# Performance work log

Hardware: AMD Instinct MI355X
Metric: run time of the kernel (lower is better)

## Reference

```python
import jax, jax.numpy as jnp
import numpy as np

BATCH = 1
SEQ = 2048
HIDDEN = 2048
NUM_HEADS = 16
NUM_KV_HEADS = 4
HEAD_DIM = HIDDEN // NUM_HEADS  # 128
KV_GROUPS = NUM_HEADS // NUM_KV_HEADS  # 4
MIN_WIN, MAX_WIN = 64, 512


def _adaptive_window_mask(key):
    # Per-query adaptive window size in [MIN_WIN, MAX_WIN); causal + windowed.
    win = jax.random.randint(key, (SEQ,), MIN_WIN, MAX_WIN)  # [S]
    i = jnp.arange(SEQ)[:, None]  # query pos
    j = jnp.arange(SEQ)[None, :]  # key pos
    mask = (j <= i) & (j > i - win[:, None])  # diagonal always True
    return jnp.broadcast_to(mask[None, None], (BATCH, 1, SEQ, SEQ))


def setup_inputs() -> dict:
    key = jax.random.key(0)
    ks = jax.random.split(key, 6)
    std = 0.02
    return {
        "hidden_states": jax.random.normal(ks[0], (BATCH, SEQ, HIDDEN), jnp.float32),
        "attention_mask": _adaptive_window_mask(ks[1]),
        "Wq": jax.random.normal(ks[2], (HIDDEN, NUM_HEADS * HEAD_DIM), jnp.float32) * std,
        "Wk": jax.random.normal(ks[3], (HIDDEN, NUM_KV_HEADS * HEAD_DIM), jnp.float32) * std,
        "Wv": jax.random.normal(ks[4], (HIDDEN, NUM_KV_HEADS * HEAD_DIM), jnp.float32) * std,
        "Wo": jax.random.normal(ks[5], (NUM_HEADS * HEAD_DIM, HIDDEN), jnp.float32) * std,
    }


def reference(hidden_states, attention_mask, Wq, Wk, Wv, Wo):
    B, S, H = hidden_states.shape
    # Projections (no bias, LLaMA-style)
    q = (hidden_states @ Wq).reshape(B, S, NUM_HEADS, HEAD_DIM).transpose(0, 2, 1, 3)
    k = (hidden_states @ Wk).reshape(B, S, NUM_KV_HEADS, HEAD_DIM).transpose(0, 2, 1, 3)
    v = (hidden_states @ Wv).reshape(B, S, NUM_KV_HEADS, HEAD_DIM).transpose(0, 2, 1, 3)
    # GQA: repeat_interleave along head dim
    k = jnp.repeat(k, KV_GROUPS, axis=1)  # [B, NUM_HEADS, S, D]
    v = jnp.repeat(v, KV_GROUPS, axis=1)
    scale = 1.0 / np.sqrt(HEAD_DIM).astype(np.float32)
    scores = jnp.einsum("bhqd,bhkd->bhqk", q, k) * scale  # [B, H, S, S]
    # bool mask: masked positions get -inf (matches masked_fill_(-inf) + add)
    scores = jnp.where(attention_mask, scores, -jnp.inf)
    attn = jax.nn.softmax(scores, axis=-1)
    out = jnp.einsum("bhqk,bhkd->bhqd", attn, v)
    out = out.transpose(0, 2, 1, 3).reshape(B, S, H) @ Wo
    return out
```

## Files before the change

kernel.cpp:

```cpp
#include <hip/hip_runtime.h>
#include <hip/hip_bf16.h>

typedef __attribute__((ext_vector_type(4)))  float f32x4;
typedef __attribute__((ext_vector_type(16))) float f32x16;
typedef __attribute__((ext_vector_type(8)))  short bf16x8;
typedef unsigned short u16;
typedef unsigned int   u32;
typedef unsigned long long u64;
typedef __attribute__((ext_vector_type(2))) u32 u32x2;
typedef __attribute__((ext_vector_type(4))) u32 u32x4;

#define S_LEN 2048
#define HID   2048
#define NH    16
#define NKV   4
#define HD    128
#define DKV   512
#define QK_SCALE 0.08838834764831845f

__device__ __forceinline__ u16 f2bf(float x) {
    u32 u = __builtin_bit_cast(u32, x);
    u32 r = (u + 0x7fffu + ((u >> 16) & 1u)) >> 16;
    return (u16)r;
}
__device__ __forceinline__ float bf2f(u16 b) {
    u32 u = ((u32)b) << 16;
    return __builtin_bit_cast(float, u);
}
__device__ __forceinline__ void gload_lds16(const void* g, void* l) {
    __builtin_amdgcn_global_load_lds(
        (const __attribute__((address_space(1))) u32*)g,
        (__attribute__((address_space(3))) u32*)l, 16, 0, 0);
}
__device__ __forceinline__ u32x4 pack8(const u16* o) {
    u32x4 r;
    r[0] = (u32)o[0] | ((u32)o[1] << 16);
    r[1] = (u32)o[2] | ((u32)o[3] << 16);
    r[2] = (u32)o[4] | ((u32)o[5] << 16);
    r[3] = (u32)o[6] | ((u32)o[7] << 16);
    return r;
}

__device__ __forceinline__ void plswap(u32 a, u32 b, u32& x0, u32& x1) {
#if __has_builtin(__builtin_amdgcn_permlane32_swap)
    u32x2 r = __builtin_amdgcn_permlane32_swap(a, b, false, false);
    x0 = r[0]; x1 = r[1];
#else
    u32 oa = (u32)__shfl_xor((int)a, 32);
    u32 ob = (u32)__shfl_xor((int)b, 32);
    int hi = (threadIdx.x & 63) >> 5;
    x0 = hi ? ob : a;
    x1 = hi ? b : oa;
#endif
}
__device__ __forceinline__ float pairmax32(float v) {
    u32 x0, x1; plswap(__builtin_bit_cast(u32, v), __builtin_bit_cast(u32, v), x0, x1);
    return fmaxf(__builtin_bit_cast(float, x0), __builtin_bit_cast(float, x1));
}
__device__ __forceinline__ float pairsum32(float v) {
    u32 x0, x1; plswap(__builtin_bit_cast(u32, v), __builtin_bit_cast(u32, v), x0, x1);
    return __builtin_bit_cast(float, x0) + __builtin_bit_cast(float, x1);
}

#define NTQ 1024
#define NTK 256
#define NTV 256
#define NTO 1024
#define NT_W (NTQ + NTK + NTV + NTO)
#define NB_CVT 1024
#define NB_START 128
#define NB_PREP (NT_W + NB_CVT + NB_START)

__global__ __launch_bounds__(256) void prep_kernel(
        const u32* __restrict__ X, const unsigned char* __restrict__ mask,
        const void* __restrict__ Wq, const void* __restrict__ Wk,
        const void* __restrict__ Wv, const void* __restrict__ Wo,
        u16* __restrict__ Xbf, u16* __restrict__ WqT, u16* __restrict__ WkT,
        u16* __restrict__ WvT, u16* __restrict__ WoT, int* __restrict__ start)
{
    __shared__ float tile[64][65];
    const int tid = threadIdx.x, lane = tid & 63, wave = tid >> 6;

    int big = 0, nz = 0;
    #pragma unroll
    for (int i = 0; i < 4; i++) {
        u32 v = X[lane + i * 64];
        u16 lo = (u16)(v & 0xffffu);
        int e = (lo >> 7) & 0xff;
        big |= (e >= 0x83);
        nz  |= (lo != 0);
    }
    const int isf32 = (__ballot(big) != 0ull || __ballot(nz) == 0ull) ? 1 : 0;

    const int b = blockIdx.x;
    if (b < NT_W) {
        const void* src; u16* dst; int N, ty;
        if (b < NTQ)                  { src = Wq; dst = WqT; N = 2048; ty = b; }
        else if (b < NTQ + NTK)       { src = Wk; dst = WkT; N = 512;  ty = b - NTQ; }
        else if (b < NTQ + NTK + NTV) { src = Wv; dst = WvT; N = 512;  ty = b - NTQ - NTK; }
        else                          { src = Wo; dst = WoT; N = 2048; ty = b - NTQ - NTK - NTV; }
        const int K = 2048;
        const int ntx = N >> 6;
        const int k0 = (ty / ntx) << 6, n0 = (ty % ntx) << 6;
        const int kk = tid >> 4, cg = (tid & 15) << 2;
        if (isf32) {
            const float* W = (const float*)src;
            #pragma unroll
            for (int it = 0; it < 4; it++) {
                f32x4 v = *(const f32x4*)(W + (size_t)(k0 + kk + it * 16) * N + n0 + cg);
                tile[kk + it * 16][cg + 0] = v[0]; tile[kk + it * 16][cg + 1] = v[1];
                tile[kk + it * 16][cg + 2] = v[2]; tile[kk + it * 16][cg + 3] = v[3];
            }
        } else {
            const u16* W = (const u16*)src;
            #pragma unroll
            for (int it = 0; it < 4; it++) {
                u64 v = *(const u64*)(W + (size_t)(k0 + kk + it * 16) * N + n0 + cg);
                tile[kk + it * 16][cg + 0] = bf2f((u16)(v));
                tile[kk + it * 16][cg + 1] = bf2f((u16)(v >> 16));
                tile[kk + it * 16][cg + 2] = bf2f((u16)(v >> 32));
                tile[kk + it * 16][cg + 3] = bf2f((u16)(v >> 48));
            }
        }
        __syncthreads();
        const int nn = tid >> 2;
        #pragma unroll
        for (int it = 0; it < 2; it++) {
            int kof = ((tid & 3) + it * 4) << 3;
            u16 ob[8];
            #pragma unroll
            for (int j = 0; j < 8; j++) ob[j] = f2bf(tile[kof + j][nn]);
            *(u32x4*)(dst + (size_t)(n0 + nn) * K + k0 + kof) = pack8(ob);
        }
    } else if (b < NT_W + NB_CVT) {
        const long base = ((long)(b - NT_W) * 256 + tid) * 16;
        u16 ob[16];
        if (isf32) {
            const float* p = (const float*)X;
            #pragma unroll
            for (int c = 0; c < 4; c++) {
                f32x4 v = *(const f32x4*)(p + base + c * 4);
                ob[c * 4 + 0] = f2bf(v[0]); ob[c * 4 + 1] = f2bf(v[1]);
                ob[c * 4 + 2] = f2bf(v[2]); ob[c * 4 + 3] = f2bf(v[3]);
            }
        } else {
            const u16* p = (const u16*)X;
            #pragma unroll
            for (int j = 0; j < 16; j++) ob[j] = p[base + j];
        }
        *(u32x4*)(Xbf + base) = pack8(ob);
        *(u32x4*)(Xbf + base + 8) = pack8(ob + 8);
    } else {
        const int b3 = b - NT_W - NB_CVT;
        const bool w1 = (mask[2049] != 0);
        #pragma unroll
        for (int rr = 0; rr < 4; rr++) {
            const int r = b3 * 16 + wave * 4 + rr;
            int cnt = 0;
            if (w1) {
                const u32* row = (const u32*)(mask + (size_t)r * S_LEN);
                #pragma unroll
                for (int i = 0; i < 8; i++) {
                    u32 v = row[lane + i * 64];
                    cnt += (int)(((v & 0x01010101u) * 0x01010101u) >> 24);
                }
            } else {
                const u32* row = (const u32*)mask + (size_t)r * S_LEN;
                #pragma unroll
                for (int i = 0; i < 32; i++) cnt += (row[lane + i * 64] != 0);
            }
            #pragma unroll
            for (int off = 32; off; off >>= 1) cnt += __shfl_down(cnt, off);
            if (lane == 0) start[r] = r + 1 - cnt;
        }
    }
}

__global__ __launch_bounds__(256) void gemm_qkv_kernel(
        const u16* __restrict__ A, const u16* __restrict__ BT,
        u16* __restrict__ Qo, u16* __restrict__ Ko, u16* __restrict__ Vto)
{
    __shared__ char smem[49152];
    const int tid = threadIdx.x;
    const int wave = tid >> 6, lane = tid & 63, g = lane >> 4, q = lane & 15;
    const int wr = wave >> 1, wc = wave & 1;
    const int gx = gridDim.x, nwg = gx * gridDim.y;
    const int wg = blockIdx.x + blockIdx.y * gx;
    const int swz = (wg & 7) * (nwg >> 3) + (wg >> 3);
    const int m0 = (swz / gx) * 128, n0 = (swz % gx) * 64;
    const int K = HID;

    f32x4 acc[4][2];
    #pragma unroll
    for (int i = 0; i < 4; i++)
        #pragma unroll
        for (int j = 0; j < 2; j++) acc[i][j] = (f32x4){0.f, 0.f, 0.f, 0.f};

    auto stage = [&](int kt, int b) {
        const int kbase = kt << 6;
        #pragma unroll
        for (int it = 0; it < 4; ++it) {
            int idx = it * 256 + tid;
            int row = idx >> 3, ch = idx & 7;
            int sch = ch ^ (row & 7);
            gload_lds16(A + (size_t)(m0 + row) * K + kbase + sch * 8,
                        smem + b * 16384 + idx * 16);
        }
        #pragma unroll
        for (int it = 0; it < 2; ++it) {
            int idx = it * 256 + tid;
            int row = idx >> 3, ch = idx & 7;
            int sch = ch ^ (row & 7);
            gload_lds16(BT + (size_t)(n0 + row) * K + kbase + sch * 8,
                        smem + 32768 + b * 8192 + idx * 16);
        }
    };

    const int KT = K >> 6;
    stage(0, 0);
    __syncthreads();
    int cur = 0;
    for (int kt = 0; kt < KT; ++kt) {
        if (kt + 1 < KT) stage(kt + 1, cur ^ 1);
        const char* sa = smem + cur * 16384;
        const char* sb = smem + 32768 + cur * 8192;
        #pragma unroll
        for (int kk = 0; kk < 2; ++kk) {
            bf16x8 af[4], bfr[2];
            #pragma unroll
            for (int i = 0; i < 4; i++) {
                int ra = wr * 64 + i * 16 + q;
                af[i] = *(const bf16x8*)(sa + ra * 128 + (((kk * 4 + g) ^ (ra & 7)) * 16));
            }
            #pragma unroll
            for (int j = 0; j < 2; j++) {
                int rb = wc * 32 + j * 16 + q;
                bfr[j] = *(const bf16x8*)(sb + rb * 128 + (((kk * 4 + g) ^ (rb & 7)) * 16));
            }
            #pragma unroll
            for (int i = 0; i < 4; i++)
                #pragma unroll
                for (int j = 0; j < 2; j++)
                    acc[i][j] = __builtin_amdgcn_mfma_f32_16x16x32_bf16(af[i], bfr[j], acc[i][j], 0, 0, 0);
        }
        __syncthreads();
        cur ^= 1;
    }
    #pragma unroll
    for (int i = 0; i < 4; i++) {
        #pragma unroll
        for (int j = 0; j < 2; j++) {
            #pragma unroll
            for (int r = 0; r < 4; r++) {
                int m = m0 + wr * 64 + i * 16 + g * 4 + r;
                int n = n0 + wc * 32 + j * 16 + q;
                float v = acc[i][j][r];
                if (n0 < 2048)      Qo[(size_t)m * HID + n] = f2bf(v * QK_SCALE);
                else if (n0 < 2560) Ko[(size_t)m * DKV + (n - 2048)] = f2bf(v);
                else                Vto[(size_t)(n - 2560) * S_LEN + m] = f2bf(v);
            }
        }
    }
}

template <int MODE>
__global__ __launch_bounds__(256) void gemm_bt_kernel(
        const u16* __restrict__ A, const u16* __restrict__ BT, void* __restrict__ Cv,
        int M, int N, int K, float scale)
{
    __shared__ char smem[49152];
    const int tid = threadIdx.x;
    const int wave = tid >> 6, lane = tid & 63, g = lane >> 4, q = lane & 15;
    const int wr = wave >> 1, wc = wave & 1;
    const int gx = gridDim.x, nwg = gx * gridDim.y;
    const int wg = blockIdx.x + blockIdx.y * gx;
    const int swz = (nwg & 7) == 0 ? ((wg & 7) * (nwg >> 3) + (wg >> 3)) : wg;
    const int m0 = (swz / gx) * 128, n0 = (swz % gx) * 64;

    f32x4 acc[4][2];
    #pragma unroll
    for (int i = 0; i < 4; i++)
        #pragma unroll
        for (int j = 0; j < 2; j++) acc[i][j] = (f32x4){0.f, 0.f, 0.f, 0.f};

    auto stage = [&](int kt, int b) {
        const int kbase = kt << 6;
        #pragma unroll
        for (int it = 0; it < 4; ++it) {
            int idx = it * 256 + tid;
            int row = idx >> 3, ch = idx & 7;
            int sch = ch ^ (row & 7);
            gload_lds16(A + (size_t)(m0 + row) * K + kbase + sch * 8,
                        smem + b * 16384 + idx * 16);
        }
        #pragma unroll
        for (int it = 0; it < 2; ++it) {
            int idx = it * 256 + tid;
            int row = idx >> 3, ch = idx & 7;
            int sch = ch ^ (row & 7);
            gload_lds16(BT + (size_t)(n0 + row) * K + kbase + sch * 8,
                        smem + 32768 + b * 8192 + idx * 16);
        }
    };

    const int KT = K >> 6;
    stage(0, 0);
    __syncthreads();
    int cur = 0;
    for (int kt = 0; kt < KT; ++kt) {
        if (kt + 1 < KT) stage(kt + 1, cur ^ 1);
        const char* sa = smem + cur * 16384;
        const char* sb = smem + 32768 + cur * 8192;
        #pragma unroll
        for (int kk = 0; kk < 2; ++kk) {
            bf16x8 af[4], bfr[2];
            #pragma unroll
            for (int i = 0; i < 4; i++) {
                int ra = wr * 64 + i * 16 + q;
                af[i] = *(const bf16x8*)(sa + ra * 128 + (((kk * 4 + g) ^ (ra & 7)) * 16));
            }
            #pragma unroll
            for (int j = 0; j < 2; j++) {
                int rb = wc * 32 + j * 16 + q;
                bfr[j] = *(const bf16x8*)(sb + rb * 128 + (((kk * 4 + g) ^ (rb & 7)) * 16));
            }
            #pragma unroll
            for (int i = 0; i < 4; i++)
                #pragma unroll
                for (int j = 0; j < 2; j++)
                    acc[i][j] = __builtin_amdgcn_mfma_f32_16x16x32_bf16(af[i], bfr[j], acc[i][j], 0, 0, 0);
        }
        __syncthreads();
        cur ^= 1;
    }
    #pragma unroll
    for (int i = 0; i < 4; i++) {
        #pragma unroll
        for (int j = 0; j < 2; j++) {
            #pragma unroll
            for (int r = 0; r < 4; r++) {
                int m = m0 + wr * 64 + i * 16 + g * 4 + r;
                int n = n0 + wc * 32 + j * 16 + q;
                float v = acc[i][j][r] * scale;
                if (MODE == 3) ((float*)Cv)[(size_t)m * N + n] = v;
                else           ((u16*)Cv)[(size_t)m * N + n] = f2bf(v);
            }
        }
    }
}

__global__ __launch_bounds__(256, 1) void attn_kernel(
        const u16* __restrict__ Q, const u16* __restrict__ Kb,
        const u16* __restrict__ Vt, u16* __restrict__ O, const int* __restrict__ start)
{
    const int tid = threadIdx.x, wave = tid >> 6, lane = tid & 63;
    const int q = lane & 31, hi = lane >> 5;
    const int h = blockIdx.y, hk = h >> 2;
    const int r0 = blockIdx.x * 128 + wave * 32;
    const int qrow = r0 + q;

    const u16* qp = Q + (size_t)qrow * HID + h * HD + hi * 8;
    bf16x8 Qf[8];
    #pragma unroll
    for (int kc = 0; kc < 8; kc++) Qf[kc] = *(const bf16x8*)(qp + kc * 16);

    const int startq = start[qrow];
    int jlo = startq;
    #pragma unroll
    for (int off = 1; off < 32; off <<= 1) jlo = min(jlo, __shfl_xor(jlo, off));
    const int jend = r0 + 31;

    float m = -INFINITY, l = 0.f;
    f32x16 o[4];
    #pragma unroll
    for (int dt = 0; dt < 4; dt++) o[dt] = (f32x16){};

    for (int j0 = (jlo & ~31); j0 <= jend; j0 += 32) {
        const u16* kp = Kb + (size_t)(j0 + q) * DKV + hk * HD + hi * 8;
        bf16x8 Kf[8];
        #pragma unroll
        for (int kc = 0; kc < 8; kc++) Kf[kc] = *(const bf16x8*)(kp + kc * 16);
        const u16* vp = Vt + (size_t)(hk * HD + q) * S_LEN + j0 + hi * 8;
        bf16x8 Vf[8];
        #pragma unroll
        for (int dt = 0; dt < 4; dt++)
            #pragma unroll
            for (int c = 0; c < 2; c++)
                Vf[dt * 2 + c] = *(const bf16x8*)(vp + (size_t)dt * 32 * S_LEN + c * 16);

        f32x16 s = (f32x16){};
        #pragma unroll
        for (int kc = 0; kc < 8; kc++)
            s = __builtin_amdgcn_mfma_f32_32x32x16_bf16(Kf[kc], Qf[kc], s, 0, 0, 0);

        float sv[16];
        float pmax = -INFINITY;
        #pragma unroll
        for (int r = 0; r < 16; r++) {
            int j = j0 + (r & 3) + 8 * (r >> 2) + 4 * hi;
            float x = (j <= qrow && j >= startq) ? s[r] : -INFINITY;
            sv[r] = x;
            pmax = fmaxf(pmax, x);
        }
        pmax = pairmax32(pmax);

        bool defer = __all(pmax <= m + 8.f);
        float mnew = m;
        if (!defer) {
            mnew = fmaxf(m, pmax);
            float corr = (m == -INFINITY) ? 0.f : __expf(m - mnew);
            l *= corr;
            #pragma unroll
            for (int dt = 0; dt < 4; dt++)
                #pragma unroll
                for (int r = 0; r < 16; r++) o[dt][r] *= corr;
            m = mnew;
        }

        float ps = 0.f;
        u16 pb[16];
        #pragma unroll
        for (int r = 0; r < 16; r++) {
            float p = (sv[r] == -INFINITY) ? 0.f : __expf(sv[r] - mnew);
            ps += p;
            pb[r] = f2bf(p);
        }
        l += pairsum32(ps);

        u32 w[8];
        #pragma unroll
        for (int i = 0; i < 8; i++) w[i] = (u32)pb[2 * i] | ((u32)pb[2 * i + 1] << 16);
        u32 x0, x1, y0, y1;
        plswap(w[0], w[2], x0, x1); plswap(w[1], w[3], y0, y1);
        u32x4 c0w = {x0, y0, x1, y1};
        bf16x8 P0 = __builtin_bit_cast(bf16x8, c0w);
        plswap(w[4], w[6], x0, x1); plswap(w[5], w[7], y0, y1);
        u32x4 c1w = {x0, y0, x1, y1};
        bf16x8 P1 = __builtin_bit_cast(bf16x8, c1w);

        #pragma unroll
        for (int dt = 0; dt < 4; dt++) {
            o[dt] = __builtin_amdgcn_mfma_f32_32x32x16_bf16(Vf[dt * 2 + 0], P0, o[dt], 0, 0, 0);
            o[dt] = __builtin_amdgcn_mfma_f32_32x32x16_bf16(Vf[dt * 2 + 1], P1, o[dt], 0, 0, 0);
        }
    }

    float inv = 1.0f / l;
    u16* op = O + (size_t)qrow * HID + h * HD + 4 * hi;
    #pragma unroll
    for (int dt = 0; dt < 4; dt++) {
        #pragma unroll
        for (int rb = 0; rb < 16; rb += 4) {
            u64 wd = (u64)f2bf(o[dt][rb + 0] * inv) |
                     ((u64)f2bf(o[dt][rb + 1] * inv) << 16) |
                     ((u64)f2bf(o[dt][rb + 2] * inv) << 32) |
                     ((u64)f2bf(o[dt][rb + 3] * inv) << 48);
            *(u64*)(op + dt * 32 + 2 * rb) = wd;
        }
    }
}

extern "C" void kernel_launch(void* const* d_in, const int* in_sizes, int n_in,
                              void* d_out, int out_size, void* d_ws, size_t ws_size,
                              hipStream_t stream)
{
    char* ws = (char*)d_ws;
    const size_t MB = 1024 * 1024;
    int* start = (int*)(ws + 1024);
    u16* Xbf = (u16*)(ws + 16384);
    u16* WqT = (u16*)(ws + 16384 + 8 * MB);
    u16* WkT = (u16*)(ws + 16384 + 16 * MB);
    u16* WvT = (u16*)(ws + 16384 + 18 * MB);
    u16* WoT = (u16*)(ws + 16384 + 20 * MB);
    u16* Qbf = (u16*)(ws + 16384 + 28 * MB);
    u16* Kbf = (u16*)(ws + 16384 + 36 * MB);
    u16* Vtb = (u16*)(ws + 16384 + 38 * MB);
    u16* Obf = (u16*)(ws + 16384 + 40 * MB);

    const void* X  = d_in[0];
    const unsigned char* mask = (const unsigned char*)d_in[1];
    const void* Wq = d_in[2];
    const void* Wk = d_in[3];
    const void* Wv = d_in[4];
    const void* Wo = d_in[5];

    prep_kernel<<<NB_PREP, 256, 0, stream>>>(
        (const u32*)X, mask, Wq, Wk, Wv, Wo, Xbf, WqT, WkT, WvT, WoT, start);

    gemm_qkv_kernel<<<dim3(48, HID / 128), 256, 0, stream>>>(Xbf, WqT, Qbf, Kbf, Vtb);

    attn_kernel<<<dim3(S_LEN / 128, NH), 256, 0, stream>>>(Qbf, Kbf, Vtb, Obf, start);

    gemm_bt_kernel<3><<<dim3(HID / 64, S_LEN / 128), 256, 0, stream>>>(Obf, WoT, d_out, S_LEN, HID, HID, 1.f);
}
```

Before: 118.3 us.

## Triple-buffer LDS in GEMM kernels with vmcnt-based partial waits

Moves the QKV and output-projection GEMMs from double to triple buffering in LDS, prefetching two K-tiles ahead. The full __syncthreads drain is replaced by s_waitcnt vmcnt(6) plus a raw barrier, so the next tile's loads stay in flight while the current tile is computed. This is meant to hide global-load latency better. In exchange, LDS per workgroup grows from 48KB to 72KB, which can cut occupancy, and correctness now depends on the hand-counted outstanding loads per stage.

```diff
diff --git a/kernel.cpp b/kernel.cpp
--- a/kernel.cpp
+++ b/kernel.cpp
@@ -180,7 +180,7 @@
         const u16* __restrict__ A, const u16* __restrict__ BT,
         u16* __restrict__ Qo, u16* __restrict__ Ko, u16* __restrict__ Vto)
 {
-    __shared__ char smem[49152];
+    __shared__ char smem[73728];
     const int tid = threadIdx.x;
     const int wave = tid >> 6, lane = tid & 63, g = lane >> 4, q = lane & 15;
     const int wr = wave >> 1, wc = wave & 1;
@@ -212,18 +212,12 @@
             int row = idx >> 3, ch = idx & 7;
             int sch = ch ^ (row & 7);
             gload_lds16(BT + (size_t)(n0 + row) * K + kbase + sch * 8,
-                        smem + 32768 + b * 8192 + idx * 16);
+                        smem + 49152 + b * 8192 + idx * 16);
         }
     };
-
-    const int KT = K >> 6;
-    stage(0, 0);
-    __syncthreads();
-    int cur = 0;
-    for (int kt = 0; kt < KT; ++kt) {
-        if (kt + 1 < KT) stage(kt + 1, cur ^ 1);
-        const char* sa = smem + cur * 16384;
-        const char* sb = smem + 32768 + cur * 8192;
+    auto compute = [&](int b) {
+        const char* sa = smem + b * 16384;
+        const char* sb = smem + 49152 + b * 8192;
         #pragma unroll
         for (int kk = 0; kk < 2; ++kk) {
             bf16x8 af[4], bfr[2];
@@ -243,9 +237,23 @@
                 for (int j = 0; j < 2; j++)
                     acc[i][j] = __builtin_amdgcn_mfma_f32_16x16x32_bf16(af[i], bfr[j], acc[i][j], 0, 0, 0);
         }
-        __syncthreads();
-        cur ^= 1;
-    }
+    };
+
+    const int KT = K >> 6;
+    stage(0, 0); stage(1, 1);
+    asm volatile("s_waitcnt vmcnt(6)" ::: "memory");
+    __builtin_amdgcn_s_barrier();
+    for (int kt = 0; kt < KT - 2; ++kt) {
+        stage(kt + 2, (kt + 2) % 3);
+        compute(kt % 3);
+        asm volatile("s_waitcnt vmcnt(6)" ::: "memory");
+        __builtin_amdgcn_s_barrier();
+    }
+    compute((KT - 2) % 3);
+    asm volatile("s_waitcnt vmcnt(0)" ::: "memory");
+    __builtin_amdgcn_s_barrier();
+    compute((KT - 1) % 3);
+
     #pragma unroll
     for (int i = 0; i < 4; i++) {
         #pragma unroll
@@ -268,7 +276,7 @@
         const u16* __restrict__ A, const u16* __restrict__ BT, void* __restrict__ Cv,
         int M, int N, int K, float scale)
 {
-    __shared__ char smem[49152];
+    __shared__ char smem[73728];
     const int tid = threadIdx.x;
     const int wave = tid >> 6, lane = tid & 63, g = lane >> 4, q = lane & 15;
     const int wr = wave >> 1, wc = wave & 1;
@@ -299,18 +307,12 @@
             int row = idx >> 3, ch = idx & 7;
             int sch = ch ^ (row & 7);
             gload_lds16(BT + (size_t)(n0 + row) * K + kbase + sch * 8,
-                        smem + 32768 + b * 8192 + idx * 16);
+                        smem + 49152 + b * 8192 + idx * 16);
         }
     };
-
-    const int KT = K >> 6;
-    stage(0, 0);
-    __syncthreads();
-    int cur = 0;
-    for (int kt = 0; kt < KT; ++kt) {
-        if (kt + 1 < KT) stage(kt + 1, cur ^ 1);
-        const char* sa = smem + cur * 16384;
-        const char* sb = smem + 32768 + cur * 8192;
+    auto compute = [&](int b) {
+        const char* sa = smem + b * 16384;
+        const char* sb = smem + 49152 + b * 8192;
         #pragma unroll
         for (int kk = 0; kk < 2; ++kk) {
             bf16x8 af[4], bfr[2];
@@ -330,9 +332,23 @@
                 for (int j = 0; j < 2; j++)
                     acc[i][j] = __builtin_amdgcn_mfma_f32_16x16x32_bf16(af[i], bfr[j], acc[i][j], 0, 0, 0);
         }
-        __syncthreads();
-        cur ^= 1;
-    }
+    };
+
+    const int KT = K >> 6;
+    stage(0, 0); stage(1, 1);
+    asm volatile("s_waitcnt vmcnt(6)" ::: "memory");
+    __builtin_amdgcn_s_barrier();
+    for (int kt = 0; kt < KT - 2; ++kt) {
+        stage(kt + 2, (kt + 2) % 3);
+        compute(kt % 3);
+        asm volatile("s_waitcnt vmcnt(6)" ::: "memory");
+        __builtin_amdgcn_s_barrier();
+    }
+    compute((KT - 2) % 3);
+    asm volatile("s_waitcnt vmcnt(0)" ::: "memory");
+    __builtin_amdgcn_s_barrier();
+    compute((KT - 1) % 3);
+
     #pragma unroll
     for (int i = 0; i < 4; i++) {
         #pragma unroll
```

Measured after the change: 122.7 us. 1.04x slower.

## Load QKV GEMM B operand directly into registers, bypassing LDS

Applied to the files above, without the earlier changes.

The QKV projection GEMM no longer stages the weight (B) tile through shared memory. Each wave loads its B fragments straight from global memory into registers, double-buffered in two register sets, while A is still staged through LDS. The main loop is unrolled by two to alternate between the register buffers. This cuts LDS footprint from 48KB to 32KB and removes the B-side LDS writes and reads, which may raise occupancy. In exchange it adds register pressure, and each B row is fetched by both waves sharing the same wc, doubling global B traffic through cache.

```diff
diff --git a/kernel.cpp b/kernel.cpp
--- a/kernel.cpp
+++ b/kernel.cpp
@@ -180,7 +180,7 @@
         const u16* __restrict__ A, const u16* __restrict__ BT,
         u16* __restrict__ Qo, u16* __restrict__ Ko, u16* __restrict__ Vto)
 {
-    __shared__ char smem[49152];
+    __shared__ char smem[32768];
     const int tid = threadIdx.x;
     const int wave = tid >> 6, lane = tid & 63, g = lane >> 4, q = lane & 15;
     const int wr = wave >> 1, wc = wave & 1;
@@ -196,7 +196,9 @@
         #pragma unroll
         for (int j = 0; j < 2; j++) acc[i][j] = (f32x4){0.f, 0.f, 0.f, 0.f};
 
-    auto stage = [&](int kt, int b) {
+    const u16* bbase = BT + (size_t)(n0 + wc * 32 + q) * K + g * 8;
+
+    auto stageA = [&](int kt, int b) {
         const int kbase = kt << 6;
         #pragma unroll
         for (int it = 0; it < 4; ++it) {
@@ -206,46 +208,49 @@
             gload_lds16(A + (size_t)(m0 + row) * K + kbase + sch * 8,
                         smem + b * 16384 + idx * 16);
         }
-        #pragma unroll
-        for (int it = 0; it < 2; ++it) {
-            int idx = it * 256 + tid;
-            int row = idx >> 3, ch = idx & 7;
-            int sch = ch ^ (row & 7);
-            gload_lds16(BT + (size_t)(n0 + row) * K + kbase + sch * 8,
-                        smem + 32768 + b * 8192 + idx * 16);
-        }
     };
-
-    const int KT = K >> 6;
-    stage(0, 0);
-    __syncthreads();
-    int cur = 0;
-    for (int kt = 0; kt < KT; ++kt) {
-        if (kt + 1 < KT) stage(kt + 1, cur ^ 1);
-        const char* sa = smem + cur * 16384;
-        const char* sb = smem + 32768 + cur * 8192;
+    auto loadB = [&](int kt, bf16x8 (&B)[2][2]) {
+        const int kbase = kt << 6;
+        #pragma unroll
+        for (int j = 0; j < 2; j++)
+            #pragma unroll
+            for (int kk = 0; kk < 2; kk++)
+                B[j][kk] = *(const bf16x8*)(bbase + (size_t)j * 16 * K + kbase + kk * 32);
+    };
+    auto compute = [&](int b, const bf16x8 (&B)[2][2]) {
+        const char* sa = smem + b * 16384;
         #pragma unroll
         for (int kk = 0; kk < 2; ++kk) {
-            bf16x8 af[4], bfr[2];
+            bf16x8 af[4];
             #pragma unroll
             for (int i = 0; i < 4; i++) {
                 int ra = wr * 64 + i * 16 + q;
                 af[i] = *(const bf16x8*)(sa + ra * 128 + (((kk * 4 + g) ^ (ra & 7)) * 16));
             }
             #pragma unroll
-            for (int j = 0; j < 2; j++) {
-                int rb = wc * 32 + j * 16 + q;
-                bfr[j] = *(const bf16x8*)(sb + rb * 128 + (((kk * 4 + g) ^ (rb & 7)) * 16));
-            }
-            #pragma unroll
             for (int i = 0; i < 4; i++)
                 #pragma unroll
                 for (int j = 0; j < 2; j++)
-                    acc[i][j] = __builtin_amdgcn_mfma_f32_16x16x32_bf16(af[i], bfr[j], acc[i][j], 0, 0, 0);
-        }
+                    acc[i][j] = __builtin_amdgcn_mfma_f32_16x16x32_bf16(af[i], B[j][kk], acc[i][j], 0, 0, 0);
+        }
+    };
+
+    bf16x8 BA[2][2], BB[2][2];
+    const int KT = K >> 6;
+    loadB(0, BA);
+    stageA(0, 0);
+    __syncthreads();
+    for (int kt = 0; kt < KT; kt += 2) {
+        if (kt + 1 < KT) { loadB(kt + 1, BB); stageA(kt + 1, 1); }
+        compute(0, BA);
         __syncthreads();
-        cur ^= 1;
-    }
+        if (kt + 2 < KT) { loadB(kt + 2, BA); stageA(kt + 2, 0); }
+        if (kt + 1 < KT) {
+            compute(1, BB);
+            __syncthreads();
+        }
+    }
+
     #pragma unroll
     for (int i = 0; i < 4; i++) {
         #pragma unroll
```

Result: slower. 148.7 us (+25.7%).

## Store Q/K/V in MFMA fragment-major layout for contiguous attention loads

Applied to the files above, without the earlier changes.

The QKV GEMM epilogue now writes Q, K and V straight into a per-head, per-32-row-tile fragment layout that matches the register fragments the attention MFMA loop consumes. Each lane then loads one contiguous 16-byte chunk, and a wave reads a fully contiguous 1 KB block per fragment instead of strided rows. This removes uncoalesced, strided global loads in the attention inner loop, especially for V, which was read across the sequence stride. The cost is scattered 2-byte stores in the GEMM epilogue, which may write less efficiently.

```diff
diff --git a/kernel.cpp b/kernel.cpp
--- a/kernel.cpp
+++ b/kernel.cpp
@@ -178,7 +178,7 @@
 
 __global__ __launch_bounds__(256) void gemm_qkv_kernel(
         const u16* __restrict__ A, const u16* __restrict__ BT,
-        u16* __restrict__ Qo, u16* __restrict__ Ko, u16* __restrict__ Vto)
+        u16* __restrict__ Qf, u16* __restrict__ Kf, u16* __restrict__ Vf)
 {
     __shared__ char smem[49152];
     const int tid = threadIdx.x;
@@ -255,9 +255,26 @@
                 int m = m0 + wr * 64 + i * 16 + g * 4 + r;
                 int n = n0 + wc * 32 + j * 16 + q;
                 float v = acc[i][j][r];
-                if (n0 < 2048)      Qo[(size_t)m * HID + n] = f2bf(v * QK_SCALE);
-                else if (n0 < 2560) Ko[(size_t)m * DKV + (n - 2048)] = f2bf(v);
-                else                Vto[(size_t)(n - 2560) * S_LEN + m] = f2bf(v);
+                int t = m >> 5, jj = m & 31;
+                if (n0 < 2048) {
+                    int h = n >> 7, dd = n & 127;
+                    int kc = dd >> 4, hi8 = (dd >> 3) & 1, e = dd & 7;
+                    Qf[(size_t)h * 262144 + t * 4096 + kc * 512 + (jj + hi8 * 32) * 8 + e]
+                        = f2bf(v * QK_SCALE);
+                } else if (n0 < 2560) {
+                    int d = n - 2048;
+                    int hkk = d >> 7, dd = d & 127;
+                    int kc = dd >> 4, hi8 = (dd >> 3) & 1, e = dd & 7;
+                    Kf[(size_t)hkk * 262144 + t * 4096 + kc * 512 + (jj + hi8 * 32) * 8 + e]
+                        = f2bf(v);
+                } else {
+                    int d = n - 2560;
+                    int hkk = d >> 7, dd = d & 127;
+                    int dt = dd >> 5, l31 = dd & 31;
+                    int c = (jj >> 4) & 1, hi8 = (jj >> 3) & 1, e = jj & 7;
+                    Vf[(size_t)hkk * 262144 + t * 4096 + (dt * 2 + c) * 512 + (l31 + hi8 * 32) * 8 + e]
+                        = f2bf(v);
+                }
             }
         }
     }
@@ -359,10 +376,10 @@
     const int r0 = blockIdx.x * 128 + wave * 32;
     const int qrow = r0 + q;
 
-    const u16* qp = Q + (size_t)qrow * HID + h * HD + hi * 8;
+    const u16* qf = Q + (size_t)h * 262144 + (r0 >> 5) * 4096 + lane * 8;
     bf16x8 Qf[8];
     #pragma unroll
-    for (int kc = 0; kc < 8; kc++) Qf[kc] = *(const bf16x8*)(qp + kc * 16);
+    for (int kc = 0; kc < 8; kc++) Qf[kc] = *(const bf16x8*)(qf + kc * 512);
 
     const int startq = start[qrow];
     int jlo = startq;
@@ -375,18 +392,19 @@
     #pragma unroll
     for (int dt = 0; dt < 4; dt++) o[dt] = (f32x16){};
 
+    const u16* kfb = Kb + (size_t)hk * 262144 + lane * 8;
+    const u16* vfb = Vt + (size_t)hk * 262144 + lane * 8;
+
     for (int j0 = (jlo & ~31); j0 <= jend; j0 += 32) {
-        const u16* kp = Kb + (size_t)(j0 + q) * DKV + hk * HD + hi * 8;
+        const int t = j0 >> 5;
+        const u16* kf = kfb + t * 4096;
         bf16x8 Kf[8];
         #pragma unroll
-        for (int kc = 0; kc < 8; kc++) Kf[kc] = *(const bf16x8*)(kp + kc * 16);
-        const u16* vp = Vt + (size_t)(hk * HD + q) * S_LEN + j0 + hi * 8;
+        for (int kc = 0; kc < 8; kc++) Kf[kc] = *(const bf16x8*)(kf + kc * 512);
+        const u16* vf = vfb + t * 4096;
         bf16x8 Vf[8];
         #pragma unroll
-        for (int dt = 0; dt < 4; dt++)
-            #pragma unroll
-            for (int c = 0; c < 2; c++)
-                Vf[dt * 2 + c] = *(const bf16x8*)(vp + (size_t)dt * 32 * S_LEN + c * 16);
+        for (int idx = 0; idx < 8; idx++) Vf[idx] = *(const bf16x8*)(vf + idx * 512);
 
         f32x16 s = (f32x16){};
         #pragma unroll
@@ -472,9 +490,9 @@
     u16* WkT = (u16*)(ws + 16384 + 16 * MB);
     u16* WvT = (u16*)(ws + 16384 + 18 * MB);
     u16* WoT = (u16*)(ws + 16384 + 20 * MB);
-    u16* Qbf = (u16*)(ws + 16384 + 28 * MB);
-    u16* Kbf = (u16*)(ws + 16384 + 36 * MB);
-    u16* Vtb = (u16*)(ws + 16384 + 38 * MB);
+    u16* Qfr = (u16*)(ws + 16384 + 28 * MB);
+    u16* Kfr = (u16*)(ws + 16384 + 36 * MB);
+    u16* Vfr = (u16*)(ws + 16384 + 38 * MB);
     u16* Obf = (u16*)(ws + 16384 + 40 * MB);
 
     const void* X  = d_in[0];
@@ -487,9 +505,9 @@
     prep_kernel<<<NB_PREP, 256, 0, stream>>>(
         (const u32*)X, mask, Wq, Wk, Wv, Wo, Xbf, WqT, WkT, WvT, WoT, start);
 
-    gemm_qkv_kernel<<<dim3(48, HID / 128), 256, 0, stream>>>(Xbf, WqT, Qbf, Kbf, Vtb);
-
-    attn_kernel<<<dim3(S_LEN / 128, NH), 256, 0, stream>>>(Qbf, Kbf, Vtb, Obf, start);
+    gemm_qkv_kernel<<<dim3(48, HID / 128), 256, 0, stream>>>(Xbf, WqT, Qfr, Kfr, Vfr);
+
+    attn_kernel<<<dim3(S_LEN / 128, NH), 256, 0, stream>>>(Qfr, Kfr, Vfr, Obf, start);
 
     gemm_bt_kernel<3><<<dim3(HID / 64, S_LEN / 128), 256, 0, stream>>>(Obf, WoT, d_out, S_LEN, HID, HID, 1.f);
 }
```

Measured after the change: 106.6 us. 9.9% less time.
